# Kernel optimization log

Hardware: AMD Instinct MI355X
Metric: run time of the kernel (lower is better)

Reference implementation:

```python
import jax, jax.numpy as jnp
import numpy as np

B, C, H, W = 4, 512, 64, 64


def setup_inputs() -> dict:
    key = jax.random.key(0)
    kq, kk, kv = jax.random.split(key, 3)
    query = jax.random.normal(kq, (B, C, H, W), dtype=jnp.float32)
    key_t = jax.random.normal(kk, (B, C, H, W), dtype=jnp.float32)
    value = jax.random.normal(kv, (B, C, H, W), dtype=jnp.float32)
    return {"query": query, "key": key_t, "value": value}


def reference(query, key, value):
    # num_convs=0 -> convs is Identity; normalize=False; use_residual=True
    b, c, h, w = query.shape
    n = h * w
    q = query.reshape(b, c, n)   # [B, C, N]
    k = key.reshape(b, c, n)     # [B, C, N]
    v = value.reshape(b, c, n)   # [B, C, N]
    # affinity[b, i, j] = sum_c k[b, c, i] * q[b, c, j]
    affinity = jnp.einsum('bci,bcj->bij', k, q)
    # softmax over dim=1 (the key index i)
    affinity = jax.nn.softmax(affinity, axis=1)
    # out = value @ affinity : [B, C, N] x [B, N, N] -> [B, C, N]
    out = jnp.einsum('bci,bij->bcj', v, affinity)
    out = out.reshape(b, c, h, w)
    return out + query
```

## Files before the change

kernel.cpp:

```cpp
#include <hip/hip_runtime.h>
#include <math.h>

typedef __attribute__((ext_vector_type(4))) float f32x4;
typedef __attribute__((ext_vector_type(8))) short bf16x8;
typedef _Float16 f16x8 __attribute__((ext_vector_type(8)));

namespace {
constexpr int B_ = 4, C_ = 512, N_ = 4096;
constexpr float MFIX = 96.0f;
}

__device__ __forceinline__ unsigned short f2bf(float f) {
    unsigned int u = __float_as_uint(f);
    u = (u + 0x7fffu + ((u >> 16) & 1u)) >> 16;
    return (unsigned short)u;
}
__device__ __forceinline__ float bf2f(unsigned short h) {
    return __uint_as_float(((unsigned int)h) << 16);
}
__device__ __forceinline__ unsigned short f2h(float f) {
    return __builtin_bit_cast(unsigned short, (_Float16)f);
}
__device__ __forceinline__ float h2f(unsigned short u) {
    return (float)__builtin_bit_cast(_Float16, u);
}
__device__ __forceinline__ void gll16(const unsigned short* g, unsigned short* l) {
    __builtin_amdgcn_global_load_lds(
        (const __attribute__((address_space(1))) void*)g,
        (__attribute__((address_space(3))) void*)l, 16, 0, 0);
}

__global__ __launch_bounds__(256)
void cvt_k_cat(const float* __restrict__ X, unsigned short* __restrict__ Kc)
{
    __shared__ float tile[64][66];
    const int t   = (int)threadIdx.x;
    const int blk = (int)blockIdx.x;
    const int b   = blk >> 9;
    const int r   = blk & 511;
    const int it  = r >> 3;
    const int ct  = r & 7;

    const float* src = X + ((size_t)(b * C_ + ct * 64)) * N_ + it * 64;
    #pragma unroll
    for (int rep = 0; rep < 4; ++rep) {
        int idx = rep * 256 + t;
        int c   = idx >> 4;
        int i4  = (idx & 15) * 4;
        const float4 v = *(const float4*)(src + (size_t)c * N_ + i4);
        tile[c][i4 + 0] = v.x; tile[c][i4 + 1] = v.y;
        tile[c][i4 + 2] = v.z; tile[c][i4 + 3] = v.w;
    }
    __syncthreads();
    unsigned short* dh = Kc + ((size_t)(b * N_ + it * 64)) * 1024 + ct * 64;
    #pragma unroll
    for (int rep = 0; rep < 4; ++rep) {
        int idx = rep * 256 + t;
        int i   = idx >> 4;
        int c4  = (idx & 15) * 4;
        ushort4 hv, lv;
        {
            float f0 = tile[c4 + 0][i], f1 = tile[c4 + 1][i];
            float f2 = tile[c4 + 2][i], f3 = tile[c4 + 3][i];
            hv.x = f2h(f0); lv.x = f2h(f0 - h2f(hv.x));
            hv.y = f2h(f1); lv.y = f2h(f1 - h2f(hv.y));
            hv.z = f2h(f2); lv.z = f2h(f2 - h2f(hv.z));
            hv.w = f2h(f3); lv.w = f2h(f3 - h2f(hv.w));
        }
        *(ushort4*)(dh + (size_t)i * 1024 + c4)       = hv;
        *(ushort4*)(dh + (size_t)i * 1024 + 512 + c4) = lv;
    }
}

__global__ __launch_bounds__(256)
void cvt_transpose_hi_f16(const float* __restrict__ X,
                          unsigned short* __restrict__ Xh)
{
    __shared__ float tile[64][66];
    const int t   = (int)threadIdx.x;
    const int blk = (int)blockIdx.x;
    const int b   = blk >> 9;
    const int r   = blk & 511;
    const int it  = r >> 3;
    const int ct  = r & 7;

    const float* src = X + ((size_t)(b * C_ + ct * 64)) * N_ + it * 64;
    #pragma unroll
    for (int rep = 0; rep < 4; ++rep) {
        int idx = rep * 256 + t;
        int c   = idx >> 4;
        int i4  = (idx & 15) * 4;
        const float4 v = *(const float4*)(src + (size_t)c * N_ + i4);
        tile[c][i4 + 0] = v.x; tile[c][i4 + 1] = v.y;
        tile[c][i4 + 2] = v.z; tile[c][i4 + 3] = v.w;
    }
    __syncthreads();
    unsigned short* dh = Xh + ((size_t)(b * N_ + it * 64)) * C_ + ct * 64;
    #pragma unroll
    for (int rep = 0; rep < 4; ++rep) {
        int idx = rep * 256 + t;
        int i   = idx >> 4;
        int c4  = (idx & 15) * 4;
        ushort4 hv;
        hv.x = f2h(tile[c4 + 0][i]);
        hv.y = f2h(tile[c4 + 1][i]);
        hv.z = f2h(tile[c4 + 2][i]);
        hv.w = f2h(tile[c4 + 3][i]);
        *(ushort4*)(dh + (size_t)i * C_ + c4) = hv;
    }
}

__global__ __launch_bounds__(256)
void cvt_split_hi(const float* __restrict__ X, unsigned short* __restrict__ Xh)
{
    size_t base = ((size_t)blockIdx.x * 256 + threadIdx.x) * 16;
    #pragma unroll
    for (int g = 0; g < 2; ++g) {
        float4 a = *(const float4*)(X + base + g * 8);
        float4 c = *(const float4*)(X + base + g * 8 + 4);
        ushort4 h0, h1;
        h0.x = f2bf(a.x); h0.y = f2bf(a.y); h0.z = f2bf(a.z); h0.w = f2bf(a.w);
        h1.x = f2bf(c.x); h1.y = f2bf(c.y); h1.z = f2bf(c.z); h1.w = f2bf(c.w);
        *(ushort4*)(Xh + base + g * 8)     = h0;
        *(ushort4*)(Xh + base + g * 8 + 4) = h1;
    }
}

__global__ __launch_bounds__(512, 4)
void gemm1_exp(const unsigned short* __restrict__ Kcat,
               const unsigned short* __restrict__ Qth,
               unsigned short* __restrict__ Pp,
               float* __restrict__ colpart,
               int b0)
{
    __shared__ char ldsc[49152];

    const int t    = (int)threadIdx.x;
    const int w    = t >> 6;
    const int lane = t & 63;
    const int lr   = lane & 15;
    const int lg   = lane >> 4;
    const int wr   = w >> 1;
    const int wc   = w & 1;

    const int q8   = (int)gridDim.x >> 3;
    const int wg   = ((int)blockIdx.x & 7) * q8 + ((int)blockIdx.x >> 3);
    const int slot = wg >> 9;
    const int wl   = wg & 511;
    const int ti   = wl >> 5;
    const int tj   = wl & 31;
    const int b    = b0 + slot;
    const int bN   = b * N_;

    Pp      += (size_t)slot * N_ * N_;
    colpart += (size_t)slot * 16 * N_;

    int offA[4], offB[4];
    #pragma unroll
    for (int m = 0; m < 4; ++m) {
        const int i = wr * 64 + m * 16 + lr, mi = i >> 1;
        offA[m] = mi * 128 + (((((i & 1) << 2) + lg) ^ (mi & 7)) << 4);
    }
    #pragma unroll
    for (int n = 0; n < 4; ++n) {
        const int j = wc * 64 + n * 16 + lr, mj = j >> 1;
        offB[n] = mj * 128 + (((((j & 1) << 2) + lg) ^ (mj & 7)) << 4);
    }

    const unsigned short* srcP[3];
    int dstO[3], dStep[3];
    bool isA[3];
    #pragma unroll
    for (int r = 0; r < 3; ++r) {
        const int c = w * 3 + r;
        if (c < 16) {
            const int qg = c * 64 + lane;
            const int m_ = qg >> 3;
            const int qr = (qg & 7) ^ (m_ & 7);
            srcP[r] = Kcat + ((size_t)(bN + ti * 256 + 2 * m_ + (qr >> 2))) * 1024 + (qr & 3) * 8;
            dstO[r] = c * 1024;
            dStep[r] = 16384;
            isA[r] = true;
        } else {
            const int g  = c - 16;
            const int qg = g * 64 + lane;
            const int m_ = qg >> 3;
            const int qr = (qg & 7) ^ (m_ & 7);
            srcP[r] = Qth + ((size_t)(bN + tj * 128 + 2 * m_ + (qr >> 2))) * 512 + (qr & 3) * 8;
            dstO[r] = 32768 + g * 1024;
            dStep[r] = 8192;
            isA[r] = false;
        }
    }
    auto stage = [&](int d, int sn) {
        #pragma unroll
        for (int r = 0; r < 3; ++r) {
            const int off = (isA[r] ? sn : (sn & 15)) * 32;
            gll16(srcP[r] + off, (unsigned short*)(ldsc + dstO[r] + d * dStep[r]));
        }
    };

    f32x4 acc[4][4];
    #pragma unroll
    for (int x = 0; x < 4; ++x)
        #pragma unroll
        for (int y = 0; y < 4; ++y) acc[x][y] = (f32x4)0.0f;

    stage(0, 0);
    __syncthreads();

    #pragma unroll 2
    for (int s = 0; s < 32; ++s) {
        if (s + 1 < 32) stage((s + 1) & 1, s + 1);
        const char* Ac = ldsc + (s & 1) * 16384;
        const char* Bc = ldsc + 32768 + (s & 1) * 8192;
        f16x8 af[4], bfv[4];
        #pragma unroll
        for (int m = 0; m < 4; ++m) af[m] = *(const f16x8*)(Ac + offA[m]);
        #pragma unroll
        for (int n = 0; n < 4; ++n) bfv[n] = *(const f16x8*)(Bc + offB[n]);
        __builtin_amdgcn_s_setprio(1);
        #pragma unroll
        for (int m = 0; m < 4; ++m)
            #pragma unroll
            for (int n = 0; n < 4; ++n)
                acc[m][n] = __builtin_amdgcn_mfma_f32_16x16x32_f16(af[m], bfv[n], acc[m][n], 0, 0, 0);
        __builtin_amdgcn_s_setprio(0);
        __syncthreads();
    }

    unsigned short* Ptmp = (unsigned short*)ldsc;
    float* red = (float*)(ldsc + 33280);

    #pragma unroll
    for (int n = 0; n < 4; ++n) {
        float cs = 0.0f;
        #pragma unroll
        for (int m = 0; m < 4; ++m) {
            acc[m][n][0] = __expf(acc[m][n][0] - MFIX);
            acc[m][n][1] = __expf(acc[m][n][1] - MFIX);
            acc[m][n][2] = __expf(acc[m][n][2] - MFIX);
            acc[m][n][3] = __expf(acc[m][n][3] - MFIX);
            cs += (acc[m][n][0] + acc[m][n][1]) + (acc[m][n][2] + acc[m][n][3]);
        }
        cs += __shfl_xor(cs, 16);
        cs += __shfl_xor(cs, 32);
        if (lane < 16) red[wr * 128 + wc * 64 + n * 16 + lane] = cs;
    }

    if (wc == 0) {
        #pragma unroll
        for (int n = 0; n < 4; ++n) {
            const int jl = n * 16 + lr;
            #pragma unroll
            for (int m = 0; m < 4; ++m) {
                ushort4 pk;
                pk.x = f2bf(acc[m][n][0]); pk.y = f2bf(acc[m][n][1]);
                pk.z = f2bf(acc[m][n][2]); pk.w = f2bf(acc[m][n][3]);
                *(ushort4*)(Ptmp + jl * 260 + wr * 64 + m * 16 + lg * 4) = pk;
            }
        }
    }
    __syncthreads();

    if (t < 128)
        colpart[(size_t)ti * N_ + tj * 128 + t] =
            (red[t] + red[128 + t]) + (red[256 + t] + red[384 + t]);
    {
        const int j   = t >> 3;
        const int seg = (t & 7) * 32;
        const unsigned short* sp = Ptmp + j * 260 + seg;
        unsigned short* dp = Pp + (size_t)(tj * 128 + j) * N_ + ti * 256 + seg;
        #pragma unroll
        for (int k2 = 0; k2 < 4; ++k2)
            *(uint4*)(dp + k2 * 8) = *(const uint4*)(sp + k2 * 8);
    }
    __syncthreads();

    if (wc == 1) {
        #pragma unroll
        for (int n = 0; n < 4; ++n) {
            const int jl = n * 16 + lr;
            #pragma unroll
            for (int m = 0; m < 4; ++m) {
                ushort4 pk;
                pk.x = f2bf(acc[m][n][0]); pk.y = f2bf(acc[m][n][1]);
                pk.z = f2bf(acc[m][n][2]); pk.w = f2bf(acc[m][n][3]);
                *(ushort4*)(Ptmp + jl * 260 + wr * 64 + m * 16 + lg * 4) = pk;
            }
        }
    }
    __syncthreads();

    {
        const int j   = t >> 3;
        const int seg = (t & 7) * 32;
        const unsigned short* sp = Ptmp + j * 260 + seg;
        unsigned short* dp = Pp + (size_t)(tj * 128 + 64 + j) * N_ + ti * 256 + seg;
        #pragma unroll
        for (int k2 = 0; k2 < 4; ++k2)
            *(uint4*)(dp + k2 * 8) = *(const uint4*)(sp + k2 * 8);
    }
}

__global__ __launch_bounds__(256, 2)
void gemm2_out(const unsigned short* __restrict__ Vb,
               const unsigned short* __restrict__ Pp,
               const float* __restrict__ colpart,
               const float* __restrict__ Qorig,
               float* __restrict__ Out,
               int b0, int nwg)
{
    __shared__ char ldsc[49152];

    const int t    = (int)threadIdx.x;
    const int w    = t >> 6;
    const int lane = t & 63;
    const int lr   = lane & 15;
    const int lg   = lane >> 4;

    const int q8 = nwg >> 3;
    const int wg = ((int)blockIdx.x & 7) * q8 + ((int)blockIdx.x >> 3);
    const int pb = wg >> 8;
    const int wl = wg & 255;
    const int tc = wl >> 6;
    const int tj = wl & 63;
    const int b  = b0 + pb;

    const unsigned short* aP = Vb + (size_t)(b * C_ + tc * 128) * N_;
    const unsigned short* bP = Pp + (size_t)pb * N_ * N_ + (size_t)(tj * 64) * N_;
    const float* cpb = colpart + (size_t)pb * 16 * N_;

    int offA[2][2], offB[4][2];
    #pragma unroll
    for (int x = 0; x < 2; ++x) {
        const int ar = w * 32 + x * 16 + lr;
        #pragma unroll
        for (int ks = 0; ks < 2; ++ks)
            offA[x][ks] = ar * 128 + (((ks * 4 + lg) ^ (ar & 7)) << 4);
    }
    #pragma unroll
    for (int x = 0; x < 4; ++x) {
        const int br = x * 16 + lr;
        #pragma unroll
        for (int ks = 0; ks < 2; ++ks)
            offB[x][ks] = br * 128 + (((ks * 4 + lg) ^ (br & 7)) << 4);
    }

    const int rl    = lane >> 3;
    const int qlog8 = ((lane & 7) ^ rl) * 8;
    auto stage = [&](int d, int coff) {
        unsigned short* Ad = (unsigned short*)(ldsc + d * 16384);
        unsigned short* Bd = (unsigned short*)(ldsc + 32768 + d * 8192);
        #pragma unroll
        for (int r = 0; r < 4; ++r) {
            const int q = w + r * 4;
            gll16(aP + (size_t)(q * 8 + rl) * N_ + coff + qlog8, Ad + q * 512);
        }
        #pragma unroll
        for (int r = 0; r < 2; ++r) {
            const int q = w * 2 + r;
            gll16(bP + (size_t)(q * 8 + rl) * N_ + coff + qlog8, Bd + q * 512);
        }
    };

    f32x4 acc[2][4];
    #pragma unroll
    for (int x = 0; x < 2; ++x)
        #pragma unroll
        for (int y = 0; y < 4; ++y) acc[x][y] = (f32x4)0.0f;

    stage(0, 0);
    __syncthreads();

    #pragma unroll 2
    for (int s = 0; s < 64; ++s) {
        if (s + 1 < 64) stage((s + 1) & 1, (s + 1) * 64);
        const char* Ac = ldsc + (s & 1) * 16384;
        const char* Bc = ldsc + 32768 + (s & 1) * 8192;
        #pragma unroll
        for (int ks = 0; ks < 2; ++ks) {
            bf16x8 af[2], bfv[4];
            #pragma unroll
            for (int x = 0; x < 2; ++x) af[x] = *(const bf16x8*)(Ac + offA[x][ks]);
            #pragma unroll
            for (int x = 0; x < 4; ++x) bfv[x] = *(const bf16x8*)(Bc + offB[x][ks]);
            #pragma unroll
            for (int it = 0; it < 2; ++it)
                #pragma unroll
                for (int jt = 0; jt < 4; ++jt)
                    acc[it][jt] = __builtin_amdgcn_mfma_f32_16x16x32_bf16(
                        af[it], bfv[jt], acc[it][jt], 0, 0, 0);
        }
        __syncthreads();
    }

    float* linv = (float*)ldsc;
    if (t < 64) {
        float l = 0.0f;
        #pragma unroll 4
        for (int tt = 0; tt < 16; ++tt) l += cpb[(size_t)tt * N_ + tj * 64 + t];
        linv[t] = 1.0f / l;
    }
    __syncthreads();
    float il[4];
    #pragma unroll
    for (int jt = 0; jt < 4; ++jt) il[jt] = linv[jt * 16 + lr];
    #pragma unroll
    for (int it = 0; it < 2; ++it) {
        #pragma unroll
        for (int r = 0; r < 4; ++r) {
            const int c = tc * 128 + w * 32 + it * 16 + lg * 4 + r;
            const float* qrow = Qorig + ((size_t)(b * C_ + c)) * N_ + tj * 64;
            float*       orow = Out   + ((size_t)(b * C_ + c)) * N_ + tj * 64;
            #pragma unroll
            for (int jt = 0; jt < 4; ++jt) {
                const int j = jt * 16 + lr;
                orow[j] = qrow[j] + acc[it][jt][r] * il[jt];
            }
        }
    }
}

namespace {
constexpr int FJT = 32, FIB = 64, FTPB = 256, FNJT = N_ / FJT;
}
__global__ __launch_bounds__(FTPB, 2)
void attn_fused_f32(const float* __restrict__ Q,
                    const float* __restrict__ K,
                    const float* __restrict__ V,
                    float* __restrict__ O)
{
    __shared__ float q_lds[C_][FJT];
    __shared__ float p_t[FJT][FIB + 4];
    __shared__ float red_max[8][FJT];
    __shared__ float red_sum[8][FJT];

    const int t  = (int)threadIdx.x;
    const int j  = t & (FJT - 1);
    const int g  = t >> 5;
    const int b  = (int)blockIdx.x / FNJT;
    const int j0 = ((int)blockIdx.x % FNJT) * FJT;

    const float* Qb = Q + ((size_t)b * C_) * N_ + j0;
    const float* Kb = K + ((size_t)b * C_) * N_;
    const float* Vb = V + ((size_t)b * C_) * N_;
    float*       Ob = O + ((size_t)b * C_) * N_ + j0;

    #pragma unroll 4
    for (int r = 0; r < (C_ * FJT) / FTPB; ++r) {
        int idx = r * FTPB + t;
        q_lds[idx >> 5][idx & (FJT - 1)] = Qb[(size_t)(idx >> 5) * N_ + (idx & (FJT - 1))];
    }
    __syncthreads();

    float acc[64];
    #pragma unroll
    for (int x = 0; x < 64; ++x) acc[x] = 0.0f;
    float m_run = -INFINITY, l_run = 0.0f;

    for (int i0 = 0; i0 < N_; i0 += FIB) {
        float s_acc[8];
        #pragma unroll
        for (int r = 0; r < 8; ++r) s_acc[r] = 0.0f;
        const float* kp = Kb + i0 + g * 8;
        #pragma unroll 4
        for (int c = 0; c < C_; ++c) {
            float qv = q_lds[c][j];
            const float4 k0 = *(const float4*)(kp + (size_t)c * N_);
            const float4 k1 = *(const float4*)(kp + (size_t)c * N_ + 4);
            s_acc[0] = fmaf(k0.x, qv, s_acc[0]); s_acc[1] = fmaf(k0.y, qv, s_acc[1]);
            s_acc[2] = fmaf(k0.z, qv, s_acc[2]); s_acc[3] = fmaf(k0.w, qv, s_acc[3]);
            s_acc[4] = fmaf(k1.x, qv, s_acc[4]); s_acc[5] = fmaf(k1.y, qv, s_acc[5]);
            s_acc[6] = fmaf(k1.z, qv, s_acc[6]); s_acc[7] = fmaf(k1.w, qv, s_acc[7]);
        }
        float tmax = fmaxf(fmaxf(fmaxf(s_acc[0], s_acc[1]), fmaxf(s_acc[2], s_acc[3])),
                           fmaxf(fmaxf(s_acc[4], s_acc[5]), fmaxf(s_acc[6], s_acc[7])));
        red_max[g][j] = tmax;
        __syncthreads();
        float bmax = red_max[0][j];
        #pragma unroll
        for (int gg = 1; gg < 8; ++gg) bmax = fmaxf(bmax, red_max[gg][j]);
        float new_m = fmaxf(m_run, bmax);
        float scale = __expf(m_run - new_m);
        float psum = 0.0f, pv[8];
        #pragma unroll
        for (int r = 0; r < 8; ++r) { pv[r] = __expf(s_acc[r] - new_m); psum += pv[r]; }
        #pragma unroll
        for (int r = 0; r < 8; ++r) p_t[j][g * 8 + r] = pv[r];
        red_sum[g][j] = psum;
        __syncthreads();
        float bsum = 0.0f;
        #pragma unroll
        for (int gg = 0; gg < 8; ++gg) bsum += red_sum[gg][j];
        l_run = l_run * scale + bsum;
        m_run = new_m;
        #pragma unroll
        for (int x = 0; x < 64; ++x) acc[x] *= scale;
        const float* vp = Vb + (size_t)(g * 64) * N_ + i0;
        for (int i4 = 0; i4 < 16; ++i4) {
            const float4 p4 = *(const float4*)&p_t[j][i4 * 4];
            const float* vpi = vp + i4 * 4;
            #pragma unroll
            for (int cq = 0; cq < 4; ++cq) {
                #pragma unroll
                for (int ci = 0; ci < 16; ++ci) {
                    const int cc = cq * 16 + ci;
                    const float4 vv = *(const float4*)(vpi + (size_t)cc * N_);
                    acc[cc] = fmaf(vv.x, p4.x, acc[cc]);
                    acc[cc] = fmaf(vv.y, p4.y, acc[cc]);
                    acc[cc] = fmaf(vv.z, p4.z, acc[cc]);
                    acc[cc] = fmaf(vv.w, p4.w, acc[cc]);
                }
                asm volatile("" ::: "memory");
            }
        }
    }
    const float inv_l = 1.0f / l_run;
    #pragma unroll
    for (int cc = 0; cc < 64; ++cc) {
        const int c = g * 64 + cc;
        Ob[(size_t)c * N_ + j] = q_lds[c][j] + acc[cc] * inv_l;
    }
}

extern "C" void kernel_launch(void* const* d_in, const int* in_sizes, int n_in,
                              void* d_out, int out_size, void* d_ws, size_t ws_size,
                              hipStream_t stream) {
    const float* Q = (const float*)d_in[0];
    const float* K = (const float*)d_in[1];
    const float* V = (const float*)d_in[2];
    float* O = (float*)d_out;

    const size_t EL  = (size_t)B_ * C_ * N_;
    const size_t PP1 = (size_t)N_ * N_;
    const size_t CPF = 16 * (size_t)N_;

    const size_t NEED1 = (EL * 4 + PP1) * 2 + CPF * 4;
    const size_t NEED2 = (EL * 4 + 2 * PP1) * 2 + 2 * CPF * 4;

    if (ws_size >= NEED1) {
        unsigned short* Kcat = (unsigned short*)d_ws;
        unsigned short* Qth  = Kcat + 2 * EL;
        unsigned short* Vbb  = Qth + EL;
        unsigned short* Pp   = Vbb + EL;
        const bool two = (ws_size >= NEED2);
        float* colpart = (float*)(Pp + (two ? 2 : 1) * PP1);

        cvt_k_cat<<<dim3(2048), dim3(256), 0, stream>>>(K, Kcat);
        cvt_transpose_hi_f16<<<dim3(2048), dim3(256), 0, stream>>>(Q, Qth);
        cvt_split_hi<<<dim3(2048), dim3(256), 0, stream>>>(V, Vbb);

        if (two) {
            for (int bp = 0; bp < 4; bp += 2) {
                gemm1_exp<<<dim3(1024), dim3(512), 0, stream>>>(
                    Kcat, Qth, Pp, colpart, bp);
                gemm2_out<<<dim3(512), dim3(256), 0, stream>>>(
                    Vbb, Pp, colpart, Q, O, bp, 512);
            }
        } else {
            for (int b = 0; b < 4; ++b) {
                gemm1_exp<<<dim3(512), dim3(512), 0, stream>>>(
                    Kcat, Qth, Pp, colpart, b);
                gemm2_out<<<dim3(256), dim3(256), 0, stream>>>(
                    Vbb, Pp, colpart, Q, O, b, 256);
            }
        }
    } else {
        attn_fused_f32<<<dim3(B_ * FNJT), dim3(FTPB), 0, stream>>>(Q, K, V, O);
    }
}
```

Measured before the change: 318.9 us.

## Triple-buffer LDS staging with prefetch depth two in both GEMM kernels

Both GEMM main loops move from double buffering to three LDS buffers, with global-to-LDS loads issued two stages ahead. The full __syncthreads per iteration is replaced by an explicit vmcnt wait plus a single s_barrier, so more memory latency can hide behind MFMA work. gemm2 also raises wave priority around its MFMA block. In exchange, LDS per block grows to 72KB, which may cut blocks per CU, especially for the 512-thread gemm1.

```diff
diff --git a/kernel.cpp b/kernel.cpp
--- a/kernel.cpp
+++ b/kernel.cpp
@@ -133,7 +133,7 @@
                float* __restrict__ colpart,
                int b0)
 {
-    __shared__ char ldsc[49152];
+    __shared__ char ldsc[73728];
 
     const int t    = (int)threadIdx.x;
     const int w    = t >> 6;
@@ -168,7 +168,7 @@
     }
 
     const unsigned short* srcP[3];
-    int dstO[3], dStep[3];
+    int dOff[3];
     bool isA[3];
     #pragma unroll
     for (int r = 0; r < 3; ++r) {
@@ -178,25 +178,25 @@
             const int m_ = qg >> 3;
             const int qr = (qg & 7) ^ (m_ & 7);
             srcP[r] = Kcat + ((size_t)(bN + ti * 256 + 2 * m_ + (qr >> 2))) * 1024 + (qr & 3) * 8;
-            dstO[r] = c * 1024;
-            dStep[r] = 16384;
-            isA[r] = true;
+            dOff[r] = c * 1024;
+            isA[r]  = true;
         } else {
             const int g  = c - 16;
             const int qg = g * 64 + lane;
             const int m_ = qg >> 3;
             const int qr = (qg & 7) ^ (m_ & 7);
             srcP[r] = Qth + ((size_t)(bN + tj * 128 + 2 * m_ + (qr >> 2))) * 512 + (qr & 3) * 8;
-            dstO[r] = 32768 + g * 1024;
-            dStep[r] = 8192;
-            isA[r] = false;
-        }
-    }
-    auto stage = [&](int d, int sn) {
+            dOff[r] = g * 1024;
+            isA[r]  = false;
+        }
+    }
+    auto stage = [&](int buf, int sn) {
         #pragma unroll
         for (int r = 0; r < 3; ++r) {
             const int off = (isA[r] ? sn : (sn & 15)) * 32;
-            gll16(srcP[r] + off, (unsigned short*)(ldsc + dstO[r] + d * dStep[r]));
+            char* dst = isA[r] ? (ldsc + buf * 16384 + dOff[r])
+                               : (ldsc + 49152 + buf * 8192 + dOff[r]);
+            gll16(srcP[r] + off, (unsigned short*)dst);
         }
     };
 
@@ -207,18 +207,17 @@
         for (int y = 0; y < 4; ++y) acc[x][y] = (f32x4)0.0f;
 
     stage(0, 0);
-    __syncthreads();
-
-    #pragma unroll 2
-    for (int s = 0; s < 32; ++s) {
-        if (s + 1 < 32) stage((s + 1) & 1, s + 1);
-        const char* Ac = ldsc + (s & 1) * 16384;
-        const char* Bc = ldsc + 32768 + (s & 1) * 8192;
+    stage(1, 1);
+
+    auto body = [&](int s) {
+        const char* Ac = ldsc + (s % 3) * 16384;
+        const char* Bc = ldsc + 49152 + (s % 3) * 8192;
         f16x8 af[4], bfv[4];
         #pragma unroll
         for (int m = 0; m < 4; ++m) af[m] = *(const f16x8*)(Ac + offA[m]);
         #pragma unroll
         for (int n = 0; n < 4; ++n) bfv[n] = *(const f16x8*)(Bc + offB[n]);
+        if (s + 2 < 32) stage((s + 2) % 3, s + 2);
         __builtin_amdgcn_s_setprio(1);
         #pragma unroll
         for (int m = 0; m < 4; ++m)
@@ -226,11 +225,24 @@
             for (int n = 0; n < 4; ++n)
                 acc[m][n] = __builtin_amdgcn_mfma_f32_16x16x32_f16(af[m], bfv[n], acc[m][n], 0, 0, 0);
         __builtin_amdgcn_s_setprio(0);
-        __syncthreads();
-    }
+    };
+
+    for (int s = 0; s < 31; ++s) {
+        asm volatile("s_waitcnt vmcnt(3)" ::: "memory");
+        __builtin_amdgcn_s_barrier();
+        __builtin_amdgcn_sched_barrier(0);
+        body(s);
+    }
+    {
+        asm volatile("s_waitcnt vmcnt(0)" ::: "memory");
+        __builtin_amdgcn_s_barrier();
+        __builtin_amdgcn_sched_barrier(0);
+        body(31);
+    }
+    __syncthreads();
 
     unsigned short* Ptmp = (unsigned short*)ldsc;
-    float* red = (float*)(ldsc + 33280);
+    float* red = (float*)(ldsc + 36864);
 
     #pragma unroll
     for (int n = 0; n < 4; ++n) {
@@ -311,7 +323,7 @@
                float* __restrict__ Out,
                int b0, int nwg)
 {
-    __shared__ char ldsc[49152];
+    __shared__ char ldsc[73728];
 
     const int t    = (int)threadIdx.x;
     const int w    = t >> 6;
@@ -349,9 +361,9 @@
 
     const int rl    = lane >> 3;
     const int qlog8 = ((lane & 7) ^ rl) * 8;
-    auto stage = [&](int d, int coff) {
-        unsigned short* Ad = (unsigned short*)(ldsc + d * 16384);
-        unsigned short* Bd = (unsigned short*)(ldsc + 32768 + d * 8192);
+    auto stage = [&](int buf, int coff) {
+        unsigned short* Ad = (unsigned short*)(ldsc + buf * 16384);
+        unsigned short* Bd = (unsigned short*)(ldsc + 49152 + buf * 8192);
         #pragma unroll
         for (int r = 0; r < 4; ++r) {
             const int q = w + r * 4;
@@ -371,13 +383,12 @@
         for (int y = 0; y < 4; ++y) acc[x][y] = (f32x4)0.0f;
 
     stage(0, 0);
-    __syncthreads();
-
-    #pragma unroll 2
-    for (int s = 0; s < 64; ++s) {
-        if (s + 1 < 64) stage((s + 1) & 1, (s + 1) * 64);
-        const char* Ac = ldsc + (s & 1) * 16384;
-        const char* Bc = ldsc + 32768 + (s & 1) * 8192;
+    stage(1, 64);
+
+    auto body = [&](int s) {
+        const char* Ac = ldsc + (s % 3) * 16384;
+        const char* Bc = ldsc + 49152 + (s % 3) * 8192;
+        if (s + 2 < 64) stage((s + 2) % 3, (s + 2) * 64);
         #pragma unroll
         for (int ks = 0; ks < 2; ++ks) {
             bf16x8 af[2], bfv[4];
@@ -385,15 +396,30 @@
             for (int x = 0; x < 2; ++x) af[x] = *(const bf16x8*)(Ac + offA[x][ks]);
             #pragma unroll
             for (int x = 0; x < 4; ++x) bfv[x] = *(const bf16x8*)(Bc + offB[x][ks]);
+            __builtin_amdgcn_s_setprio(1);
             #pragma unroll
             for (int it = 0; it < 2; ++it)
                 #pragma unroll
                 for (int jt = 0; jt < 4; ++jt)
                     acc[it][jt] = __builtin_amdgcn_mfma_f32_16x16x32_bf16(
                         af[it], bfv[jt], acc[it][jt], 0, 0, 0);
-        }
-        __syncthreads();
-    }
+            __builtin_amdgcn_s_setprio(0);
+        }
+    };
+
+    for (int s = 0; s < 63; ++s) {
+        asm volatile("s_waitcnt vmcnt(6)" ::: "memory");
+        __builtin_amdgcn_s_barrier();
+        __builtin_amdgcn_sched_barrier(0);
+        body(s);
+    }
+    {
+        asm volatile("s_waitcnt vmcnt(0)" ::: "memory");
+        __builtin_amdgcn_s_barrier();
+        __builtin_amdgcn_sched_barrier(0);
+        body(63);
+    }
+    __syncthreads();
 
     float* linv = (float*)ldsc;
     if (t < 64) {
```

Result: faster. 308.7 us (-3.2%).
